# Optimization experiments

Measured on AMD Instinct MI355X. Metric: run time of the kernel, lower is better.

Reference implementation:

```python
import jax, jax.numpy as jnp
import numpy as np

B, I, O, K, H = 64, 16384, 1024, 5, 16  # batch, input_dim, output_dim, num_basis, basis hidden


def setup_inputs() -> dict:
    key = jax.random.key(0)
    ks = jax.random.split(key, 6)
    x = jax.random.normal(ks[0], (B, I), dtype=jnp.float32)
    # Per-basis 1->16->1 MLP params (Linear(1,16): weight [16,1] stored squeezed as [K,16])
    w1 = jax.random.normal(ks[1], (K, H), dtype=jnp.float32) * (1.0)
    b1 = jax.random.normal(ks[2], (K, H), dtype=jnp.float32) * 0.1
    w2 = jax.random.normal(ks[3], (K, H), dtype=jnp.float32) * (1.0 / np.sqrt(H))
    b2 = jax.random.normal(ks[4], (K,), dtype=jnp.float32) * 0.1
    # KAN mixing weights [output_dim, input_dim, num_basis]
    W = jax.random.normal(ks[5], (O, I, K), dtype=jnp.float32)
    return {"x": x, "w1": w1, "b1": b1, "w2": w2, "b2": b2, "W": W}


def reference(x, w1, b1, w2, b2, W):
    # basis MLP index per input feature (cyclic reuse of the num_basis MLPs,
    # matching intended basis_functions[in_dim % num_basis])
    K_ = w1.shape[0]
    idx = jnp.arange(x.shape[1]) % K_            # [I], static
    W1, B1 = w1[idx], b1[idx]                    # [I,H]
    W2, B2 = w2[idx], b2[idx]                    # [I,H], [I]
    # basis_i(x[:, i]) = w2_i @ silu(w1_i * x + b1_i) + b2_i
    h = jax.nn.silu(x[:, :, None] * W1[None] + B1[None])   # [B,I,H]
    basis = jnp.einsum("bih,ih->bi", h, W2) + B2[None]     # [B,I]
    # out[b,o] = sum_i sum_k W[o,i,k] * basis[b,i]  (basis broadcasts over k)
    Wsum = W.sum(axis=-1)                                  # [O,I]
    return jnp.einsum("bi,oi->bo", basis, Wsum)            # [B,O]
```

## Files before the change

kernel.cpp:

```cpp
#include <hip/hip_runtime.h>
#include <hip/hip_bf16.h>

#define B_DIM 64
#define I_DIM 16384
#define O_DIM 1024
#define K_BASIS 5
#define H_DIM 16
#define IK (I_DIM * K_BASIS)

typedef __attribute__((ext_vector_type(8))) short short8;
typedef __attribute__((ext_vector_type(4))) short short4v;
typedef __attribute__((ext_vector_type(4))) float f32x4;

__global__ __launch_bounds__(256)
void basis_kernel(const float* __restrict__ x,
                  const float* __restrict__ w1,
                  const float* __restrict__ b1,
                  const float* __restrict__ w2,
                  const float* __restrict__ b2,
                  __hip_bfloat16* __restrict__ basis) {
    __shared__ float pw1[K_BASIS * H_DIM];
    __shared__ float pb1[K_BASIS * H_DIM];
    __shared__ float pw2[K_BASIS * H_DIM];
    __shared__ float pb2[K_BASIS];
    const int t = threadIdx.x;
    if (t < K_BASIS * H_DIM) {
        pw1[t] = w1[t];
        pb1[t] = b1[t];
        pw2[t] = w2[t];
        if (t < K_BASIS) pb2[t] = b2[t];
    }
    __syncthreads();

    const int gid = blockIdx.x * 256 + t;
    const int i8 = gid % (I_DIM / 8);
    const int b  = gid / (I_DIM / 8);
    const int i0 = i8 * 8;

    const float4* xp = reinterpret_cast<const float4*>(x + (size_t)b * I_DIM + i0);
    float4 xa = xp[0];
    float4 xb = xp[1];
    float xs[8] = {xa.x, xa.y, xa.z, xa.w, xb.x, xb.y, xb.z, xb.w};

    __hip_bfloat16 res[8];
#pragma unroll
    for (int j = 0; j < 8; ++j) {
        const int idx = (i0 + j) % K_BASIS;
        const float xv = xs[j];
        float acc = 0.f;
#pragma unroll
        for (int h = 0; h < H_DIM; ++h) {
            float a = fmaf(xv, pw1[idx * H_DIM + h], pb1[idx * H_DIM + h]);
            float s = a / (1.f + __expf(-a));
            acc = fmaf(s, pw2[idx * H_DIM + h], acc);
        }
        res[j] = __float2bfloat16(acc + pb2[idx]);
    }
    *reinterpret_cast<short8*>(basis + (size_t)b * I_DIM + i0) =
        *reinterpret_cast<short8*>(res);
}

#define NT 64
#define KC 160
#define NCHUNK 8
#define LDA 168

__global__ __launch_bounds__(256, 3)
void kan_gemm(const float* __restrict__ W,
              const __hip_bfloat16* __restrict__ basis,
              float* __restrict__ out) {
    __shared__ __hip_bfloat16 As[B_DIM * LDA];
    __shared__ __hip_bfloat16 Bs[NT * LDA];

    const int t    = threadIdx.x;
    const int lane = t & 63;
    const int wv   = t >> 6;
    const int o0   = blockIdx.x * NT;
    const int ik0  = blockIdx.y * (KC * NCHUNK);

    f32x4 acc[4] = {f32x4{0,0,0,0}, f32x4{0,0,0,0}, f32x4{0,0,0,0}, f32x4{0,0,0,0}};

    for (int c = 0; c < NCHUNK; ++c) {
        const int ikb = ik0 + c * KC;

#pragma unroll
        for (int r = 0; r < 10; ++r) {
            const int idx = t + r * 256;
            const int o   = idx / 40;
            const int e4  = idx - o * 40;
            const float4 v = *reinterpret_cast<const float4*>(
                W + (size_t)(o0 + o) * IK + ikb + e4 * 4);
            __hip_bfloat16 b4[4] = {__float2bfloat16(v.x), __float2bfloat16(v.y),
                                    __float2bfloat16(v.z), __float2bfloat16(v.w)};
            *reinterpret_cast<short4v*>(&Bs[o * LDA + e4 * 4]) =
                *reinterpret_cast<short4v*>(b4);
        }

        const int ib = ikb / K_BASIS;
#pragma unroll
        for (int r = 0; r < 8; ++r) {
            const int item = t + r * 256;
            const int row  = item >> 5;
            const int ic   = item & 31;
            const __hip_bfloat16 bv = basis[(size_t)row * I_DIM + ib + ic];
#pragma unroll
            for (int k = 0; k < K_BASIS; ++k)
                As[row * LDA + ic * K_BASIS + k] = bv;
        }
        __syncthreads();

        const int col  = lane & 15;
        const int kgrp = lane >> 4;
#pragma unroll
        for (int ks = 0; ks < 5; ++ks) {
            const int koff = ks * 32 + kgrp * 8;
            const short8 bf = *reinterpret_cast<const short8*>(
                &Bs[(wv * 16 + col) * LDA + koff]);
#pragma unroll
            for (int m = 0; m < 4; ++m) {
                const short8 af = *reinterpret_cast<const short8*>(
                    &As[(m * 16 + col) * LDA + koff]);
                acc[m] = __builtin_amdgcn_mfma_f32_16x16x32_bf16(af, bf, acc[m], 0, 0, 0);
            }
        }
        __syncthreads();
    }

    const int col  = lane & 15;
    const int kgrp = lane >> 4;
    const int ocol = o0 + wv * 16 + col;
#pragma unroll
    for (int m = 0; m < 4; ++m) {
#pragma unroll
        for (int j = 0; j < 4; ++j) {
            const int brow = m * 16 + kgrp * 4 + j;
            atomicAdd(&out[(size_t)brow * O_DIM + ocol], acc[m][j]);
        }
    }
}

extern "C" void kernel_launch(void* const* d_in, const int* in_sizes, int n_in,
                              void* d_out, int out_size, void* d_ws, size_t ws_size,
                              hipStream_t stream) {
    const float* x  = (const float*)d_in[0];
    const float* w1 = (const float*)d_in[1];
    const float* b1 = (const float*)d_in[2];
    const float* w2 = (const float*)d_in[3];
    const float* b2 = (const float*)d_in[4];
    const float* W  = (const float*)d_in[5];
    float* out = (float*)d_out;
    __hip_bfloat16* basis = (__hip_bfloat16*)d_ws;

    hipMemsetAsync(d_out, 0, (size_t)out_size * sizeof(float), stream);

    basis_kernel<<<dim3((B_DIM * I_DIM / 8) / 256), dim3(256), 0, stream>>>(
        x, w1, b1, w2, b2, basis);

    dim3 grid(O_DIM / NT, IK / (KC * NCHUNK));
    kan_gemm<<<grid, dim3(256), 0, stream>>>(W, basis, out);
}
```

Baseline: 101.0 us.

## Pre-sum W over basis dim in GEMM loader and prefetch next chunk in registers

The GEMM no longer expands basis values five times into the K dimension. Each thread now sums the five W entries per input while loading, so the MFMA reduction runs over I instead of I*K, which cuts MFMA work and shared-memory traffic by a factor of five. Loads for the next chunk are issued into registers before the current chunk's compute (software pipelining), and occupancy is raised to 4 blocks. Summing in fp32 before rounding to bf16 also changes numerics slightly, and the register prefetch buffer increases register pressure.

```diff
diff --git a/kernel.cpp b/kernel.cpp
--- a/kernel.cpp
+++ b/kernel.cpp
@@ -61,73 +61,84 @@
 }
 
 #define NT 64
-#define KC 160
+#define CI 32
 #define NCHUNK 8
-#define LDA 168
+#define LDB 40
 
-__global__ __launch_bounds__(256, 3)
+__global__ __launch_bounds__(256, 4)
 void kan_gemm(const float* __restrict__ W,
               const __hip_bfloat16* __restrict__ basis,
               float* __restrict__ out) {
-    __shared__ __hip_bfloat16 As[B_DIM * LDA];
-    __shared__ __hip_bfloat16 Bs[NT * LDA];
+    __shared__ __hip_bfloat16 As[B_DIM * LDB];
+    __shared__ __hip_bfloat16 Bs[NT * LDB];
 
     const int t    = threadIdx.x;
     const int lane = t & 63;
     const int wv   = t >> 6;
     const int o0   = blockIdx.x * NT;
-    const int ik0  = blockIdx.y * (KC * NCHUNK);
+    const int i00  = blockIdx.y * (CI * NCHUNK);
+
+    const int oA = t >> 3;
+    const int i4 = (t & 7) * 4;
+    const int arow = t >> 2;
+    const int ac16 = (t & 3) * 8;
+
+    const float* wp0 = W + (size_t)(o0 + oA) * IK;
+    const float* wp1 = W + (size_t)(o0 + oA + 32) * IK;
+    const __hip_bfloat16* ap = basis + (size_t)arow * I_DIM;
+
+    float4 wr[10];
+    short8 ar;
+
+    auto issue = [&](int c) {
+        const int ig = i00 + c * CI;
+        const float4* p0 = reinterpret_cast<const float4*>(wp0 + (size_t)(ig + i4) * K_BASIS);
+        const float4* p1 = reinterpret_cast<const float4*>(wp1 + (size_t)(ig + i4) * K_BASIS);
+#pragma unroll
+        for (int q = 0; q < 5; ++q) wr[q] = p0[q];
+#pragma unroll
+        for (int q = 0; q < 5; ++q) wr[5 + q] = p1[q];
+        ar = *reinterpret_cast<const short8*>(ap + ig + ac16);
+    };
+
+    auto commit = [&]() {
+#pragma unroll
+        for (int r = 0; r < 2; ++r) {
+            const float4 v0 = wr[r * 5 + 0], v1 = wr[r * 5 + 1], v2 = wr[r * 5 + 2],
+                         v3 = wr[r * 5 + 3], v4 = wr[r * 5 + 4];
+            float s0 = v0.x + v0.y + v0.z + v0.w + v1.x;
+            float s1 = v1.y + v1.z + v1.w + v2.x + v2.y;
+            float s2 = v2.z + v2.w + v3.x + v3.y + v3.z;
+            float s3 = v3.w + v4.x + v4.y + v4.z + v4.w;
+            __hip_bfloat16 b4[4] = {__float2bfloat16(s0), __float2bfloat16(s1),
+                                    __float2bfloat16(s2), __float2bfloat16(s3)};
+            *reinterpret_cast<short4v*>(&Bs[(oA + r * 32) * LDB + i4]) =
+                *reinterpret_cast<short4v*>(b4);
+        }
+        *reinterpret_cast<short8*>(&As[arow * LDB + ac16]) = ar;
+    };
 
     f32x4 acc[4] = {f32x4{0,0,0,0}, f32x4{0,0,0,0}, f32x4{0,0,0,0}, f32x4{0,0,0,0}};
+    const int col  = lane & 15;
+    const int kgrp = lane >> 4;
+    const int koff = kgrp * 8;
 
+    issue(0);
     for (int c = 0; c < NCHUNK; ++c) {
-        const int ikb = ik0 + c * KC;
-
+        commit();
+        __syncthreads();
+        if (c + 1 < NCHUNK) issue(c + 1);
+        const short8 bf = *reinterpret_cast<const short8*>(
+            &Bs[(wv * 16 + col) * LDB + koff]);
 #pragma unroll
-        for (int r = 0; r < 10; ++r) {
-            const int idx = t + r * 256;
-            const int o   = idx / 40;
-            const int e4  = idx - o * 40;
-            const float4 v = *reinterpret_cast<const float4*>(
-                W + (size_t)(o0 + o) * IK + ikb + e4 * 4);
-            __hip_bfloat16 b4[4] = {__float2bfloat16(v.x), __float2bfloat16(v.y),
-                                    __float2bfloat16(v.z), __float2bfloat16(v.w)};
-            *reinterpret_cast<short4v*>(&Bs[o * LDA + e4 * 4]) =
-                *reinterpret_cast<short4v*>(b4);
-        }
-
-        const int ib = ikb / K_BASIS;
-#pragma unroll
-        for (int r = 0; r < 8; ++r) {
-            const int item = t + r * 256;
-            const int row  = item >> 5;
-            const int ic   = item & 31;
-            const __hip_bfloat16 bv = basis[(size_t)row * I_DIM + ib + ic];
-#pragma unroll
-            for (int k = 0; k < K_BASIS; ++k)
-                As[row * LDA + ic * K_BASIS + k] = bv;
-        }
-        __syncthreads();
-
-        const int col  = lane & 15;
-        const int kgrp = lane >> 4;
-#pragma unroll
-        for (int ks = 0; ks < 5; ++ks) {
-            const int koff = ks * 32 + kgrp * 8;
-            const short8 bf = *reinterpret_cast<const short8*>(
-                &Bs[(wv * 16 + col) * LDA + koff]);
-#pragma unroll
-            for (int m = 0; m < 4; ++m) {
-                const short8 af = *reinterpret_cast<const short8*>(
-                    &As[(m * 16 + col) * LDA + koff]);
-                acc[m] = __builtin_amdgcn_mfma_f32_16x16x32_bf16(af, bf, acc[m], 0, 0, 0);
-            }
+        for (int m = 0; m < 4; ++m) {
+            const short8 af = *reinterpret_cast<const short8*>(
+                &As[(m * 16 + col) * LDB + koff]);
+            acc[m] = __builtin_amdgcn_mfma_f32_16x16x32_bf16(af, bf, acc[m], 0, 0, 0);
         }
         __syncthreads();
     }
 
-    const int col  = lane & 15;
-    const int kgrp = lane >> 4;
     const int ocol = o0 + wv * 16 + col;
 #pragma unroll
     for (int m = 0; m < 4; ++m) {
@@ -156,6 +167,6 @@
     basis_kernel<<<dim3((B_DIM * I_DIM / 8) / 256), dim3(256), 0, stream>>>(
         x, w1, b1, w2, b2, basis);
 
-    dim3 grid(O_DIM / NT, IK / (KC * NCHUNK));
+    dim3 grid(O_DIM / NT, I_DIM / (CI * NCHUNK));
     kan_gemm<<<grid, dim3(256), 0, stream>>>(W, basis, out);
 }
```

Result: faster. 88.52 us (-12.3%).
